# Performance work log

Measured on AMD Instinct MI355X. Metric: run time of the kernel, lower is better.

Reference implementation:

```python
import jax, jax.numpy as jnp
import numpy as np

N = 4096        # nodes
E = 65536       # edges (avg degree 16)
L = 64          # latent_dims
K = 256         # kernel_dims
ED = 6          # edge_dims
DEPTH = 2


def _gelu(x):
    # torch.nn.GELU / F.gelu default = exact erf form
    return jax.nn.gelu(x, approximate=False)


def setup_inputs() -> dict:
    key = jax.random.key(0)
    ks = jax.random.split(key, 12)
    u = lambda k, shape, fan: jax.random.uniform(k, shape, jnp.float32, -1.0, 1.0) / np.sqrt(fan)
    return {
        "nodes": jax.random.normal(ks[0], (N, L), jnp.float32),
        "edge_index": jax.random.randint(ks[1], (2, E), 0, N, jnp.int32),
        "edge_attr": jax.random.uniform(ks[2], (E, ED), jnp.float32),
        # DenseNet kernel MLP: ED -> K -> K -> L*L (GELU between layers)
        "W1": u(ks[3], (ED, K), ED), "b1": jnp.zeros((K,), jnp.float32),
        "W2": u(ks[4], (K, K), K),  "b2": jnp.zeros((K,), jnp.float32),
        "W3": u(ks[5], (K, L * L), K), "b3": jnp.zeros((L * L,), jnp.float32),
        # NNConv root linear (no bias) + conv bias
        "W_root": u(ks[6], (L, L), L),
        "bias": jnp.zeros((L,), jnp.float32),
    }


def reference(nodes, edge_index, edge_attr, W1, b1, W2, b2, W3, b3, W_root, bias):
    src, dst = edge_index[0], edge_index[1]
    # Edge-conditioned dynamic weights (depend only on edge_attr -> compute once)
    h = _gelu(edge_attr @ W1 + b1)          # [E, K]
    h = _gelu(h @ W2 + b2)                  # [E, K]
    W_edge = (h @ W3 + b3).reshape(E, L, L) # [E, L_in, L_out]

    def conv(x):
        msg = jnp.einsum('ei,eio->eo', x[src], W_edge)          # gather + per-edge matmul
        agg = jax.ops.segment_sum(msg, dst, num_segments=N)     # scatter-add to dst
        return agg + x @ W_root + bias

    x = nodes
    for idx in range(DEPTH):
        x = conv(x)
        if idx < DEPTH - 1:
            x = _gelu(x)
    return x
```

## Files before the change

kernel.cpp:

```cpp
#include <hip/hip_runtime.h>
#include <math.h>

#define NN 4096
#define NE 65536
#define LL 64
#define KK 256
#define ED 6
#define MAXCHUNK 8192

typedef __bf16 bf16_t;
typedef __attribute__((ext_vector_type(8))) __bf16 bf16x8;
typedef __attribute__((ext_vector_type(4))) float f32x4;

#define OFF_CNT    ((size_t)0)
#define OFF_DESC   ((size_t)16384)
#define OFF_AGG0   ((size_t)147456)
#define OFF_AGG1   ((size_t)1196032)
#define ZERO_BYTES ((size_t)2244608)
#define OFF_CURSOR ((size_t)2244608)
#define OFF_SORTED ((size_t)2260992)
#define OFF_W2R    ((size_t)2785280)
#define OFF_W3RR   ((size_t)2916352)
#define OFF_Q0     ((size_t)5013504)
#define OFF_Q1     ((size_t)6062080)
#define OFF_X1F    ((size_t)7110656)
#define OFF_X0BF   ((size_t)8159232)
#define OFF_X1BF   ((size_t)8683520)
#define OFF_H      ((size_t)9207808)
#define OFF_P      ((size_t)42762240)

__device__ __forceinline__ float gelu_f(float x) {
    return 0.5f * x * (1.0f + erff(x * 0.7071067811865476f));
}
__device__ __forceinline__ bf16_t f2bf(float x) { return (bf16_t)x; }

__global__ void k_hist(const int* __restrict__ ei, int* __restrict__ cnt) {
    int e = blockIdx.x * 256 + threadIdx.x;
    atomicAdd(&cnt[ei[e]], 1);
}

__global__ void k_scan(const int* __restrict__ cnt, int* __restrict__ cursor,
                       int4* __restrict__ descs) {
    __shared__ int pd[1024], pc[1024];
    int t = threadIdx.x;
    int deg[4]; int sd = 0, sc = 0;
#pragma unroll
    for (int j = 0; j < 4; j++) {
        deg[j] = cnt[t * 4 + j];
        sd += deg[j];
        sc += (deg[j] + 15) >> 4;
    }
    pd[t] = sd; pc[t] = sc;
    __syncthreads();
    for (int off = 1; off < 1024; off <<= 1) {
        int vd = 0, vc = 0;
        if (t >= off) { vd = pd[t - off]; vc = pc[t - off]; }
        __syncthreads();
        pd[t] += vd; pc[t] += vc;
        __syncthreads();
    }
    int rd = (t > 0) ? pd[t - 1] : 0;
    int rc = (t > 0) ? pc[t - 1] : 0;
    for (int j = 0; j < 4; j++) {
        int v = t * 4 + j, d = deg[j];
        cursor[v] = rd;
        int nch = (d + 15) >> 4;
        for (int c = 0; c < nch; c++) {
            int rem = d - c * 16;
            descs[rc + c] = make_int4(v, rd + c * 16, rem < 16 ? rem : 16, 0);
        }
        rc += nch; rd += d;
    }
}

__global__ void k_scatter(const int* __restrict__ ei, int* __restrict__ cursor,
                          int2* __restrict__ sorted) {
    int e = blockIdx.x * 256 + threadIdx.x;
    int s = ei[e], d = ei[NE + e];
    int pos = atomicAdd(&cursor[s], 1);
    sorted[pos] = make_int2(e, d);
}

__global__ void k_prep(const float* __restrict__ W2, const float* __restrict__ W3,
                       bf16_t* __restrict__ W2r, bf16_t* __restrict__ W3rr) {
    int t = blockIdx.x * 256 + threadIdx.x;
    if (t < 65536) {
        int kk = t >> 13, nn = (t >> 9) & 15, lane = (t >> 3) & 63, j = t & 7;
        int k = kk * 32 + (lane >> 4) * 8 + j;
        int n = nn * 16 + (lane & 15);
        W2r[t] = f2bf(W2[k * 256 + n]);
    }
    if (t < 1048576) {
        int f = t;
        int sn = f >> 10, ki = (f >> 9) & 1, lane = (f >> 3) & 63, jp = f & 7;
        int i = ki * 32 + (lane >> 4) * 8 + jp;
        int s = sn * 16 + (lane & 15);
        int kk = s >> 11, nn2 = (s >> 9) & 3, lane3 = (s >> 3) & 63, j3 = s & 7;
        int k = kk * 32 + (lane3 >> 4) * 8 + j3;
        int o = nn2 * 16 + (lane3 & 15);
        W3rr[f] = f2bf(W3[k * 4096 + i * 64 + o]);
    }
}

__global__ void k_mlp1(const float* __restrict__ attr, const float* __restrict__ W1,
                       const float* __restrict__ b1, bf16_t* __restrict__ a1) {
    __shared__ float sa[ED];
    int e = blockIdx.x;
    if (threadIdx.x < ED) sa[threadIdx.x] = attr[e * ED + threadIdx.x];
    __syncthreads();
    int k = threadIdx.x;
    float acc = b1[k];
#pragma unroll
    for (int j = 0; j < ED; j++) acc += sa[j] * W1[j * 256 + k];
    a1[e * 256 + k] = f2bf(gelu_f(acc));
}

__global__ void __launch_bounds__(256) k_mlp2(const bf16_t* __restrict__ a1,
                                              const bf16_t* __restrict__ W2r,
                                              const float* __restrict__ b2,
                                              bf16_t* __restrict__ h) {
    __shared__ bf16_t sB[16384];
    int tid = threadIdx.x;
    int wave = tid >> 6, lane = tid & 63, col = lane & 15, quad = lane >> 4;
    int base = blockIdx.x * 128 + wave * 32;
    bf16x8 a[2][8];
#pragma unroll
    for (int t = 0; t < 2; t++) {
        const bf16_t* arow = a1 + (size_t)(base + t * 16 + col) * 256;
#pragma unroll
        for (int kk = 0; kk < 8; kk++)
            a[t][kk] = *(const bf16x8*)(arow + kk * 32 + quad * 8);
    }
#pragma unroll 1
    for (int p = 0; p < 4; p++) {
#pragma unroll
        for (int it = 0; it < 8; it++) {
            int c = it * 256 + tid;
            int fl = c >> 6;
            int e = (c & 63) * 8;
            int kk = fl >> 2, nnl = fl & 3;
            *(bf16x8*)(sB + fl * 512 + e) =
                *(const bf16x8*)(W2r + (size_t)(kk * 16 + p * 4 + nnl) * 512 + e);
        }
        __syncthreads();
#pragma unroll
        for (int nnl = 0; nnl < 4; nnl++) {
            f32x4 acc0, acc1;
#pragma unroll
            for (int r = 0; r < 4; r++) { acc0[r] = 0.0f; acc1[r] = 0.0f; }
#pragma unroll
            for (int kk = 0; kk < 8; kk++) {
                bf16x8 b = *(const bf16x8*)(sB + (kk * 4 + nnl) * 512 + lane * 8);
                acc0 = __builtin_amdgcn_mfma_f32_16x16x32_bf16(a[0][kk], b, acc0, 0, 0, 0);
                acc1 = __builtin_amdgcn_mfma_f32_16x16x32_bf16(a[1][kk], b, acc1, 0, 0, 0);
            }
            int ncol = (p * 4 + nnl) * 16 + col;
            float bv = b2[ncol];
#pragma unroll
            for (int r = 0; r < 4; r++) {
                int row0 = base + quad * 4 + r;
                h[(size_t)row0 * 256 + ncol] = f2bf(gelu_f(acc0[r] + bv));
                h[(size_t)(row0 + 16) * 256 + ncol] = f2bf(gelu_f(acc1[r] + bv));
            }
        }
        __syncthreads();
    }
}

__global__ void k_node0(const float* __restrict__ x, const float* __restrict__ b3,
                        bf16_t* __restrict__ xbf, float* __restrict__ Q) {
    __shared__ float sx[64];
    int v = blockIdx.x, o = threadIdx.x;
    float xv = x[v * 64 + o];
    sx[o] = xv;
    xbf[v * 64 + o] = f2bf(xv);
    __syncthreads();
    float q = 0.0f;
#pragma unroll 8
    for (int i = 0; i < 64; i++) q += sx[i] * b3[i * 64 + o];
    Q[v * 64 + o] = q;
}

__global__ void __launch_bounds__(256) k_pgemm(const bf16_t* __restrict__ xbf,
                                               const bf16_t* __restrict__ W3rr,
                                               bf16_t* __restrict__ P) {
    int strip = blockIdx.x & 63;
    int rg = blockIdx.x >> 6;
    int wave = threadIdx.x >> 6, lane = threadIdx.x & 63;
    int col = lane & 15, quad = lane >> 4;
    bf16x8 b[16][2];
#pragma unroll
    for (int nn = 0; nn < 16; nn++) {
        int sn = strip * 16 + nn;
#pragma unroll
        for (int ki = 0; ki < 2; ki++)
            b[nn][ki] = *(const bf16x8*)(W3rr + (size_t)(sn * 2 + ki) * 512 + lane * 8);
    }
#pragma unroll 1
    for (int rt = 0; rt < 4; rt++) {
        int rowbase = rg * 256 + wave * 64 + rt * 16;
        const bf16_t* arow = xbf + (size_t)(rowbase + col) * 64;
        bf16x8 a0 = *(const bf16x8*)(arow + quad * 8);
        bf16x8 a1v = *(const bf16x8*)(arow + 32 + quad * 8);
#pragma unroll
        for (int nn = 0; nn < 16; nn++) {
            f32x4 acc;
#pragma unroll
            for (int r = 0; r < 4; r++) acc[r] = 0.0f;
            acc = __builtin_amdgcn_mfma_f32_16x16x32_bf16(a0, b[nn][0], acc, 0, 0, 0);
            acc = __builtin_amdgcn_mfma_f32_16x16x32_bf16(a1v, b[nn][1], acc, 0, 0, 0);
            int sn = strip * 16 + nn;
#pragma unroll
            for (int r = 0; r < 4; r++) {
                int row = rowbase + quad * 4 + r;
                P[(size_t)row * 16384 + sn * 16 + col] = f2bf(acc[r]);
            }
        }
    }
}

__global__ void __launch_bounds__(256) k_agg(const int4* __restrict__ descs,
                                             const int2* __restrict__ sorted,
                                             const bf16_t* __restrict__ h,
                                             const bf16_t* __restrict__ P,
                                             const float* __restrict__ Q,
                                             float* __restrict__ agg) {
    int chunk = blockIdx.x * 4 + (threadIdx.x >> 6);
    int lane = threadIdx.x & 63, col = lane & 15, quad = lane >> 4;
    int4 d = descs[chunk];
    int v = d.x, base = d.y, cnt = d.z;
    if (cnt == 0) return;
    int idx = base + (col < cnt ? col : 0);
    int2 ed = sorted[idx];
    int eid = ed.x, dst = ed.y;
    bool valid = (col < cnt);

    bf16x8 zero;
#pragma unroll
    for (int i = 0; i < 8; i++) zero[i] = (bf16_t)0.0f;

    bf16x8 a[8];
    const bf16_t* hrow = h + (size_t)eid * 256;
#pragma unroll
    for (int kk = 0; kk < 8; kk++) {
        bf16x8 t = *(const bf16x8*)(hrow + kk * 32 + quad * 8);
        a[kk] = valid ? t : zero;
    }
    const bf16_t* Pv = P + (size_t)v * 16384;
    f32x4 acc[4];
#pragma unroll
    for (int nn = 0; nn < 4; nn++)
#pragma unroll
        for (int r = 0; r < 4; r++) acc[nn][r] = 0.0f;
#pragma unroll 1
    for (int half = 0; half < 2; half++) {
        bf16x8 bh[16];
#pragma unroll
        for (int kk = 0; kk < 8; kk++)
#pragma unroll
            for (int ni = 0; ni < 2; ni++)
                bh[kk * 2 + ni] = *(const bf16x8*)(Pv + (size_t)(kk * 4 + half * 2 + ni) * 512 + lane * 8);
#pragma unroll
        for (int kk = 0; kk < 8; kk++)
#pragma unroll
            for (int ni = 0; ni < 2; ni++)
                acc[half * 2 + ni] = __builtin_amdgcn_mfma_f32_16x16x32_bf16(
                    a[kk], bh[kk * 2 + ni], acc[half * 2 + ni], 0, 0, 0);
    }
#pragma unroll
    for (int nn = 0; nn < 4; nn++) {
        float qv = Q[v * 64 + nn * 16 + col];
#pragma unroll
        for (int r = 0; r < 4; r++) {
            int mm = quad * 4 + r;
            int de = __shfl(dst, mm, 64);
            if (mm < cnt)
                atomicAdd(&agg[(size_t)de * 64 + nn * 16 + col], acc[nn][r] + qv);
        }
    }
}

__global__ void k_combine1(const float* __restrict__ x, const float* __restrict__ agg,
                           const float* __restrict__ Wroot, const float* __restrict__ bias,
                           const float* __restrict__ b3, float* __restrict__ x1,
                           bf16_t* __restrict__ x1bf, float* __restrict__ Q1) {
    __shared__ float sx[64], sy[64];
    int v = blockIdx.x, o = threadIdx.x;
    sx[o] = x[v * 64 + o];
    __syncthreads();
    float acc = agg[v * 64 + o] + bias[o];
#pragma unroll 8
    for (int i = 0; i < 64; i++) acc += sx[i] * Wroot[i * 64 + o];
    acc = gelu_f(acc);
    x1[v * 64 + o] = acc;
    x1bf[v * 64 + o] = f2bf(acc);
    sy[o] = acc;
    __syncthreads();
    float q = 0.0f;
#pragma unroll 8
    for (int i = 0; i < 64; i++) q += sy[i] * b3[i * 64 + o];
    Q1[v * 64 + o] = q;
}

__global__ void k_combine2(const float* __restrict__ x1, const float* __restrict__ agg,
                           const float* __restrict__ Wroot, const float* __restrict__ bias,
                           float* __restrict__ out) {
    __shared__ float sx[64];
    int v = blockIdx.x, o = threadIdx.x;
    sx[o] = x1[v * 64 + o];
    __syncthreads();
    float acc = agg[v * 64 + o] + bias[o];
#pragma unroll 8
    for (int i = 0; i < 64; i++) acc += sx[i] * Wroot[i * 64 + o];
    out[v * 64 + o] = acc;
}

extern "C" void kernel_launch(void* const* d_in, const int* in_sizes, int n_in,
                              void* d_out, int out_size, void* d_ws, size_t ws_size,
                              hipStream_t stream) {
    const float* nodes = (const float*)d_in[0];
    const int*   ei    = (const int*)d_in[1];
    const float* attr  = (const float*)d_in[2];
    const float* W1    = (const float*)d_in[3];
    const float* b1    = (const float*)d_in[4];
    const float* W2    = (const float*)d_in[5];
    const float* b2    = (const float*)d_in[6];
    const float* W3    = (const float*)d_in[7];
    const float* b3    = (const float*)d_in[8];
    const float* Wroot = (const float*)d_in[9];
    const float* bias  = (const float*)d_in[10];
    float* out = (float*)d_out;
    char* ws = (char*)d_ws;

    int*    cnt    = (int*)(ws + OFF_CNT);
    int4*   descs  = (int4*)(ws + OFF_DESC);
    float*  agg0   = (float*)(ws + OFF_AGG0);
    float*  agg1   = (float*)(ws + OFF_AGG1);
    int*    cursor = (int*)(ws + OFF_CURSOR);
    int2*   sorted = (int2*)(ws + OFF_SORTED);
    bf16_t* W2r    = (bf16_t*)(ws + OFF_W2R);
    bf16_t* W3rr   = (bf16_t*)(ws + OFF_W3RR);
    float*  Q0     = (float*)(ws + OFF_Q0);
    float*  Q1     = (float*)(ws + OFF_Q1);
    float*  x1f    = (float*)(ws + OFF_X1F);
    bf16_t* x0bf   = (bf16_t*)(ws + OFF_X0BF);
    bf16_t* x1bf   = (bf16_t*)(ws + OFF_X1BF);
    bf16_t* hbuf   = (bf16_t*)(ws + OFF_H);
    bf16_t* Pbuf   = (bf16_t*)(ws + OFF_P);
    bf16_t* a1buf  = (bf16_t*)(ws + OFF_P);

    hipMemsetAsync(ws, 0, ZERO_BYTES, stream);
    k_hist<<<NE / 256, 256, 0, stream>>>(ei, cnt);
    k_scan<<<1, 1024, 0, stream>>>(cnt, cursor, descs);
    k_scatter<<<NE / 256, 256, 0, stream>>>(ei, cursor, sorted);
    k_prep<<<4096, 256, 0, stream>>>(W2, W3, W2r, W3rr);
    k_mlp1<<<NE, 256, 0, stream>>>(attr, W1, b1, a1buf);
    k_mlp2<<<512, 256, 0, stream>>>(a1buf, W2r, b2, hbuf);
    k_node0<<<NN, 64, 0, stream>>>(nodes, b3, x0bf, Q0);
    k_pgemm<<<1024, 256, 0, stream>>>(x0bf, W3rr, Pbuf);
    k_agg<<<MAXCHUNK / 4, 256, 0, stream>>>(descs, sorted, hbuf, Pbuf, Q0, agg0);
    k_combine1<<<NN, 64, 0, stream>>>(nodes, agg0, Wroot, bias, b3, x1f, x1bf, Q1);
    k_pgemm<<<1024, 256, 0, stream>>>(x1bf, W3rr, Pbuf);
    k_agg<<<MAXCHUNK / 4, 256, 0, stream>>>(descs, sorted, hbuf, Pbuf, Q1, agg1);
    k_combine2<<<NN, 64, 0, stream>>>(x1f, agg1, Wroot, bias, out);
}
```

Before: 320.8 us.

## Use 32x32 MFMA with 32-edge chunks in aggregation and batch mlp1 edges

```diff
diff --git a/kernel.cpp b/kernel.cpp
--- a/kernel.cpp
+++ b/kernel.cpp
@@ -6,11 +6,13 @@
 #define LL 64
 #define KK 256
 #define ED 6
-#define MAXCHUNK 8192
+#define MAXSUPER 6144
 
 typedef __bf16 bf16_t;
+typedef __attribute__((ext_vector_type(4))) __bf16 bf16x4;
 typedef __attribute__((ext_vector_type(8))) __bf16 bf16x8;
 typedef __attribute__((ext_vector_type(4))) float f32x4;
+typedef __attribute__((ext_vector_type(16))) float f32x16;
 
 #define OFF_CNT    ((size_t)0)
 #define OFF_DESC   ((size_t)16384)
@@ -48,7 +50,7 @@
     for (int j = 0; j < 4; j++) {
         deg[j] = cnt[t * 4 + j];
         sd += deg[j];
-        sc += (deg[j] + 15) >> 4;
+        sc += (deg[j] + 31) >> 5;
     }
     pd[t] = sd; pc[t] = sc;
     __syncthreads();
@@ -64,10 +66,10 @@
     for (int j = 0; j < 4; j++) {
         int v = t * 4 + j, d = deg[j];
         cursor[v] = rd;
-        int nch = (d + 15) >> 4;
+        int nch = (d + 31) >> 5;
         for (int c = 0; c < nch; c++) {
-            int rem = d - c * 16;
-            descs[rc + c] = make_int4(v, rd + c * 16, rem < 16 ? rem : 16, 0);
+            int rem = d - c * 32;
+            descs[rc + c] = make_int4(v, rd + c * 32, rem < 32 ? rem : 32, 0);
         }
         rc += nch; rd += d;
     }
@@ -95,24 +97,47 @@
         int sn = f >> 10, ki = (f >> 9) & 1, lane = (f >> 3) & 63, jp = f & 7;
         int i = ki * 32 + (lane >> 4) * 8 + jp;
         int s = sn * 16 + (lane & 15);
-        int kk = s >> 11, nn2 = (s >> 9) & 3, lane3 = (s >> 3) & 63, j3 = s & 7;
-        int k = kk * 32 + (lane3 >> 4) * 8 + j3;
-        int o = nn2 * 16 + (lane3 & 15);
+        int c = s >> 9, lane3 = (s >> 3) & 63, j3 = s & 7;
+        int k = (c >> 1) * 16 + (lane3 >> 5) * 8 + j3;
+        int o = (c & 1) * 32 + (lane3 & 31);
         W3rr[f] = f2bf(W3[k * 4096 + i * 64 + o]);
     }
 }
 
-__global__ void k_mlp1(const float* __restrict__ attr, const float* __restrict__ W1,
-                       const float* __restrict__ b1, bf16_t* __restrict__ a1) {
-    __shared__ float sa[ED];
-    int e = blockIdx.x;
-    if (threadIdx.x < ED) sa[threadIdx.x] = attr[e * ED + threadIdx.x];
-    __syncthreads();
-    int k = threadIdx.x;
-    float acc = b1[k];
-#pragma unroll
-    for (int j = 0; j < ED; j++) acc += sa[j] * W1[j * 256 + k];
-    a1[e * 256 + k] = f2bf(gelu_f(acc));
+__global__ void __launch_bounds__(256) k_mlp1(const float* __restrict__ attr,
+                                              const float* __restrict__ W1,
+                                              const float* __restrict__ b1,
+                                              bf16_t* __restrict__ a1) {
+    __shared__ float sa[64 * ED];
+    int t = threadIdx.x;
+    int e0 = blockIdx.x * 64;
+    for (int i = t; i < 64 * ED; i += 256) sa[i] = attr[(size_t)e0 * ED + i];
+    int col4 = (t & 63) * 4;
+    float w[ED][4], bb[4];
+#pragma unroll
+    for (int j = 0; j < ED; j++)
+#pragma unroll
+        for (int c = 0; c < 4; c++) w[j][c] = W1[j * 256 + col4 + c];
+#pragma unroll
+    for (int c = 0; c < 4; c++) bb[c] = b1[col4 + c];
+    __syncthreads();
+    int esub = t >> 6;
+#pragma unroll 1
+    for (int eg = 0; eg < 16; eg++) {
+        int el = eg * 4 + esub;
+        float av[ED];
+#pragma unroll
+        for (int j = 0; j < ED; j++) av[j] = sa[el * ED + j];
+        bf16x4 ov;
+#pragma unroll
+        for (int c = 0; c < 4; c++) {
+            float acc = bb[c];
+#pragma unroll
+            for (int j = 0; j < ED; j++) acc += av[j] * w[j][c];
+            ov[c] = f2bf(gelu_f(acc));
+        }
+        *(bf16x4*)(a1 + (size_t)(e0 + el) * 256 + col4) = ov;
+    }
 }
 
 __global__ void __launch_bounds__(256) k_mlp2(const bf16_t* __restrict__ a1,
@@ -226,56 +251,46 @@
                                              const float* __restrict__ Q,
                                              float* __restrict__ agg) {
     int chunk = blockIdx.x * 4 + (threadIdx.x >> 6);
-    int lane = threadIdx.x & 63, col = lane & 15, quad = lane >> 4;
+    int lane = threadIdx.x & 63;
+    int row = lane & 31, khalf = lane >> 5;
     int4 d = descs[chunk];
     int v = d.x, base = d.y, cnt = d.z;
     if (cnt == 0) return;
-    int idx = base + (col < cnt ? col : 0);
-    int2 ed = sorted[idx];
+    bool valid = (row < cnt);
+    int2 ed = sorted[base + (valid ? row : 0)];
     int eid = ed.x, dst = ed.y;
-    bool valid = (col < cnt);
 
     bf16x8 zero;
 #pragma unroll
     for (int i = 0; i < 8; i++) zero[i] = (bf16_t)0.0f;
 
-    bf16x8 a[8];
+    bf16x8 a[16];
     const bf16_t* hrow = h + (size_t)eid * 256;
 #pragma unroll
-    for (int kk = 0; kk < 8; kk++) {
-        bf16x8 t = *(const bf16x8*)(hrow + kk * 32 + quad * 8);
-        a[kk] = valid ? t : zero;
+    for (int kt = 0; kt < 16; kt++) {
+        bf16x8 t = *(const bf16x8*)(hrow + kt * 16 + khalf * 8);
+        a[kt] = valid ? t : zero;
     }
     const bf16_t* Pv = P + (size_t)v * 16384;
-    f32x4 acc[4];
-#pragma unroll
-    for (int nn = 0; nn < 4; nn++)
-#pragma unroll
-        for (int r = 0; r < 4; r++) acc[nn][r] = 0.0f;
-#pragma unroll 1
-    for (int half = 0; half < 2; half++) {
-        bf16x8 bh[16];
-#pragma unroll
-        for (int kk = 0; kk < 8; kk++)
-#pragma unroll
-            for (int ni = 0; ni < 2; ni++)
-                bh[kk * 2 + ni] = *(const bf16x8*)(Pv + (size_t)(kk * 4 + half * 2 + ni) * 512 + lane * 8);
-#pragma unroll
-        for (int kk = 0; kk < 8; kk++)
-#pragma unroll
-            for (int ni = 0; ni < 2; ni++)
-                acc[half * 2 + ni] = __builtin_amdgcn_mfma_f32_16x16x32_bf16(
-                    a[kk], bh[kk * 2 + ni], acc[half * 2 + ni], 0, 0, 0);
-    }
-#pragma unroll
-    for (int nn = 0; nn < 4; nn++) {
-        float qv = Q[v * 64 + nn * 16 + col];
-#pragma unroll
-        for (int r = 0; r < 4; r++) {
-            int mm = quad * 4 + r;
-            int de = __shfl(dst, mm, 64);
-            if (mm < cnt)
-                atomicAdd(&agg[(size_t)de * 64 + nn * 16 + col], acc[nn][r] + qv);
+    f32x16 acc0, acc1;
+#pragma unroll
+    for (int r = 0; r < 16; r++) { acc0[r] = 0.0f; acc1[r] = 0.0f; }
+#pragma unroll
+    for (int kt = 0; kt < 16; kt++) {
+        bf16x8 b0 = *(const bf16x8*)(Pv + (size_t)(kt * 2 + 0) * 512 + lane * 8);
+        bf16x8 b1 = *(const bf16x8*)(Pv + (size_t)(kt * 2 + 1) * 512 + lane * 8);
+        acc0 = __builtin_amdgcn_mfma_f32_32x32x16_bf16(a[kt], b0, acc0, 0, 0, 0);
+        acc1 = __builtin_amdgcn_mfma_f32_32x32x16_bf16(a[kt], b1, acc1, 0, 0, 0);
+    }
+    float q0 = Q[v * 64 + row];
+    float q1 = Q[v * 64 + 32 + row];
+#pragma unroll
+    for (int r = 0; r < 16; r++) {
+        int mm = (r & 3) + 8 * (r >> 2) + 4 * khalf;
+        int de = __shfl(dst, mm, 64);
+        if (mm < cnt) {
+            atomicAdd(&agg[(size_t)de * 64 + row], acc0[r] + q0);
+            atomicAdd(&agg[(size_t)de * 64 + 32 + row], acc1[r] + q1);
         }
     }
 }
@@ -354,13 +369,13 @@
     k_scan<<<1, 1024, 0, stream>>>(cnt, cursor, descs);
     k_scatter<<<NE / 256, 256, 0, stream>>>(ei, cursor, sorted);
     k_prep<<<4096, 256, 0, stream>>>(W2, W3, W2r, W3rr);
-    k_mlp1<<<NE, 256, 0, stream>>>(attr, W1, b1, a1buf);
+    k_mlp1<<<NE / 64, 256, 0, stream>>>(attr, W1, b1, a1buf);
     k_mlp2<<<512, 256, 0, stream>>>(a1buf, W2r, b2, hbuf);
     k_node0<<<NN, 64, 0, stream>>>(nodes, b3, x0bf, Q0);
     k_pgemm<<<1024, 256, 0, stream>>>(x0bf, W3rr, Pbuf);
-    k_agg<<<MAXCHUNK / 4, 256, 0, stream>>>(descs, sorted, hbuf, Pbuf, Q0, agg0);
+    k_agg<<<MAXSUPER / 4, 256, 0, stream>>>(descs, sorted, hbuf, Pbuf, Q0, agg0);
     k_combine1<<<NN, 64, 0, stream>>>(nodes, agg0, Wroot, bias, b3, x1f, x1bf, Q1);
     k_pgemm<<<1024, 256, 0, stream>>>(x1bf, W3rr, Pbuf);
-    k_agg<<<MAXCHUNK / 4, 256, 0, stream>>>(descs, sorted, hbuf, Pbuf, Q1, agg1);
+    k_agg<<<MAXSUPER / 4, 256, 0, stream>>>(descs, sorted, hbuf, Pbuf, Q1, agg1);
     k_combine2<<<NN, 64, 0, stream>>>(x1f, agg1, Wroot, bias, out);
 }
```

After: 291.8 us. -9.0%, faster.
